# Kernel tuning notes

Measured on AMD Instinct MI355X. Metric: run time of the kernel, lower is better.

Reference implementation:

```python
import jax, jax.numpy as jnp
import numpy as np

D_PAIR = 128
D_BIAS = 128
N_HEAD = 4
D_HID = 32
B = 1
L = 384
EPS = 1e-5


def _layernorm(x, gamma, beta):
    m = jnp.mean(x, axis=-1, keepdims=True)
    v = jnp.var(x, axis=-1, keepdims=True)
    return (x - m) * jax.lax.rsqrt(v + EPS) * gamma + beta


def setup_inputs() -> dict:
    key = jax.random.key(0)
    ks = jax.random.split(key, 10)
    hd = N_HEAD * D_HID
    s = 0.02
    return {
        "pair": jax.random.normal(ks[0], (B, L, L, D_PAIR), jnp.float32),
        "bias": jax.random.normal(ks[1], (B, L, L, D_BIAS), jnp.float32),
        "gamma_p": jnp.ones((D_PAIR,), jnp.float32),
        "beta_p": jnp.zeros((D_PAIR,), jnp.float32),
        "gamma_b": jnp.ones((D_BIAS,), jnp.float32),
        "beta_b": jnp.zeros((D_BIAS,), jnp.float32),
        "Wq": jax.random.normal(ks[2], (D_PAIR, hd), jnp.float32) * s,
        "Wk": jax.random.normal(ks[3], (D_PAIR, hd), jnp.float32) * s,
        "Wv": jax.random.normal(ks[4], (D_PAIR, hd), jnp.float32) * s,
        "Wb": jax.random.normal(ks[5], (D_BIAS, N_HEAD), jnp.float32) * s,
        "Wg": jax.random.normal(ks[6], (D_PAIR, hd), jnp.float32) * s,
        "bg": jnp.ones((hd,), jnp.float32),
        "Wout": jax.random.normal(ks[7], (hd, D_PAIR), jnp.float32) * s,
        "bout": jnp.zeros((D_PAIR,), jnp.float32),
    }


def reference(pair, bias, gamma_p, beta_p, gamma_b, beta_b,
              Wq, Wk, Wv, Wb, Wg, bg, Wout, bout):
    h = Wb.shape[1]
    d = Wq.shape[1] // h
    Bn, Ln = pair.shape[:2]
    scaling = 1.0 / jnp.sqrt(jnp.asarray(d, pair.dtype))

    # is_row=True: attend along rows -> swap the two L axes
    pair_t = jnp.transpose(pair, (0, 2, 1, 3))
    bias_t = jnp.transpose(bias, (0, 2, 1, 3))

    pn = _layernorm(pair_t, gamma_p, beta_p)                     # [B,L,L,dp]
    q = (pn @ Wq).reshape(Bn, Ln, Ln, h, d) * scaling            # [B,n,i,h,d]
    k = (pn @ Wk).reshape(Bn, Ln, Ln, h, d) / Ln                 # [B,n,j,h,d]

    # mean-over-n biased axial attention logits: [B,i,j,h]
    attn = jnp.einsum('bnihk,bnjhk->bijh', q, k)
    attn = attn + _layernorm(bias_t, gamma_b, beta_b) @ Wb       # learned bias
    a = jax.nn.softmax(attn, axis=-2)                            # over j

    v = (pn @ Wv).reshape(Bn, Ln, Ln, h, d)                      # [B,n,j,h,d]
    o = jnp.einsum('bijh,bnjhd->bnihd', a, v).reshape(Bn, Ln, Ln, h * d)

    gate = jax.nn.sigmoid(pn @ Wg + bg)                          # [B,L,L,h*d]
    out = (gate * o) @ Wout + bout                               # [B,L,L,dp]

    return jnp.transpose(out, (0, 2, 1, 3))                      # undo is_row permute
```

## Files before the change

kernel.cpp:

```cpp
#include <hip/hip_runtime.h>

typedef unsigned short u16;
typedef unsigned int   u32;
typedef __attribute__((ext_vector_type(8))) short bf16x8;
typedef __attribute__((ext_vector_type(4))) float f32x4;

#define LL 384
#define DP 128
#define SZROW ((size_t)LL * LL)

#define SWZ(row, col) (((row) << 7) + (((((col) >> 3) ^ ((row) & 7)) << 3) | ((col) & 7)))

__device__ __forceinline__ u16 f2bf(float x) {
  u32 u = __builtin_bit_cast(u32, x);
  u = (u + 0x7FFFu + ((u >> 16) & 1u)) >> 16;
  return (u16)u;
}
__device__ __forceinline__ float bf2f(u16 h) {
  return __builtin_bit_cast(float, ((u32)h) << 16);
}
__device__ __forceinline__ uint2 pack4(float a, float b, float c, float d) {
  uint2 p;
  p.x = (u32)f2bf(a) | ((u32)f2bf(b) << 16);
  p.y = (u32)f2bf(c) | ((u32)f2bf(d) << 16);
  return p;
}

__global__ void k_prep(const float* __restrict__ Wq, const float* __restrict__ Wk,
                       const float* __restrict__ Wv, const float* __restrict__ Wg,
                       const float* __restrict__ Wout, u16* __restrict__ wbf) {
  int r = blockIdx.x, c = threadIdx.x, m = blockIdx.y;
  const float* W;
  float s = 1.0f;
  if (m == 0)      { W = Wq;  s = 0.17677669529663687f; }
  else if (m == 1) { W = Wk;  s = 1.0f / 384.0f; }
  else if (m == 2) { W = Wv; }
  else if (m == 3) { W = Wg; }
  else             { W = Wout; }
  wbf[m * DP * DP + r * DP + c] = f2bf(W[c * DP + r] * s);
}

template <int NS>
__device__ __forceinline__ void wave_gemm(const u16* __restrict__ W, const u16* pnl,
                                          int wave, int q, int r, f32x4 (&acc)[2][NS]) {
  const f32x4 FZ = {0.f, 0.f, 0.f, 0.f};
#pragma unroll
  for (int ms = 0; ms < 2; ++ms)
#pragma unroll
    for (int ns = 0; ns < NS; ++ns) acc[ms][ns] = FZ;
#pragma unroll
  for (int kc = 0; kc < 4; ++kc) {
    bf16x8 a0 = *(const bf16x8*)(W + (wave * 32 + r) * DP + kc * 32 + q * 8);
    bf16x8 a1 = *(const bf16x8*)(W + (wave * 32 + 16 + r) * DP + kc * 32 + q * 8);
#pragma unroll
    for (int ns = 0; ns < NS; ++ns) {
      bf16x8 b = *(const bf16x8*)(pnl + SWZ(ns * 16 + r, kc * 32 + q * 8));
      acc[0][ns] = __builtin_amdgcn_mfma_f32_16x16x32_bf16(a0, b, acc[0][ns], 0, 0, 0);
      acc[1][ns] = __builtin_amdgcn_mfma_f32_16x16x32_bf16(a1, b, acc[1][ns], 0, 0, 0);
    }
  }
}

__global__ __launch_bounds__(256) void k1_ln_proj(
    const float* __restrict__ pair, const float* __restrict__ gamma_p,
    const float* __restrict__ beta_p, const u16* __restrict__ wbf,
    const float* __restrict__ bg, u16* __restrict__ Qb, u16* __restrict__ Kb,
    u16* __restrict__ Vtb, u16* __restrict__ Gtb) {
  __shared__ u16 pn[64 * 128];
  __shared__ u16 T[128 * 72];
  const int ib = blockIdx.x, n = blockIdx.y;
  const int tid = threadIdx.x;
  const int lane = tid & 63, wave = tid >> 6;
  const int q = lane >> 4, r = lane & 15;
  const int l32 = lane & 31, half = lane >> 5;
  const int c0 = l32 * 4;
  const float4 gm = *(const float4*)(gamma_p + c0);
  const float4 bt = *(const float4*)(beta_p + c0);

#pragma unroll
  for (int it = 0; it < 8; ++it) {
    const int il = it * 8 + wave * 2 + half;
    const float* rowp = pair + ((size_t)(ib * 64 + il) * LL + n) * DP + c0;
    float4 x = *(const float4*)rowp;
    float s1 = x.x + x.y + x.z + x.w;
    float s2 = x.x * x.x + x.y * x.y + x.z * x.z + x.w * x.w;
#pragma unroll
    for (int m = 16; m >= 1; m >>= 1) { s1 += __shfl_xor(s1, m); s2 += __shfl_xor(s2, m); }
    float mean = s1 * (1.0f / 128.0f);
    float rs = rsqrtf(s2 * (1.0f / 128.0f) - mean * mean + 1e-5f);
    *(uint2*)(&pn[SWZ(il, c0)]) =
        pack4((x.x - mean) * rs * gm.x + bt.x, (x.y - mean) * rs * gm.y + bt.y,
              (x.z - mean) * rs * gm.z + bt.z, (x.w - mean) * rs * gm.w + bt.w);
  }
  __syncthreads();

  f32x4 acc[2][4];

  wave_gemm<4>(wbf, pn, wave, q, r, acc);
#pragma unroll
  for (int ms = 0; ms < 2; ++ms) {
    int ob = wave * 32 + ms * 16 + q * 4;
#pragma unroll
    for (int ns = 0; ns < 4; ++ns) {
      size_t base = ((size_t)n * LL + ib * 64 + ns * 16 + r) * DP + ob;
      *(uint2*)(Qb + base) = pack4(acc[ms][ns][0], acc[ms][ns][1], acc[ms][ns][2], acc[ms][ns][3]);
    }
  }
  wave_gemm<4>(wbf + DP * DP, pn, wave, q, r, acc);
#pragma unroll
  for (int ms = 0; ms < 2; ++ms) {
    int ob = wave * 32 + ms * 16 + q * 4;
#pragma unroll
    for (int ns = 0; ns < 4; ++ns) {
      size_t base = ((size_t)n * LL + ib * 64 + ns * 16 + r) * DP + ob;
      *(uint2*)(Kb + base) = pack4(acc[ms][ns][0], acc[ms][ns][1], acc[ms][ns][2], acc[ms][ns][3]);
    }
  }
  wave_gemm<4>(wbf + 2 * DP * DP, pn, wave, q, r, acc);
#pragma unroll
  for (int ms = 0; ms < 2; ++ms)
#pragma unroll
    for (int ns = 0; ns < 4; ++ns)
#pragma unroll
      for (int reg = 0; reg < 4; ++reg)
        T[(wave * 32 + ms * 16 + q * 4 + reg) * 72 + ns * 16 + r] = f2bf(acc[ms][ns][reg]);
  __syncthreads();
#pragma unroll
  for (int it = 0; it < 4; ++it) {
    int c = it * 32 + (tid >> 3);
    int il2 = (tid & 7) * 8;
    *(uint4*)(Vtb + ((size_t)n * DP + c) * LL + ib * 64 + il2) =
        *(const uint4*)(T + c * 72 + il2);
  }
  wave_gemm<4>(wbf + 3 * DP * DP, pn, wave, q, r, acc);
  __syncthreads();
#pragma unroll
  for (int ms = 0; ms < 2; ++ms) {
    f32x4 bgv = *(const f32x4*)(bg + wave * 32 + ms * 16 + q * 4);
#pragma unroll
    for (int ns = 0; ns < 4; ++ns)
#pragma unroll
      for (int reg = 0; reg < 4; ++reg) {
        float x = acc[ms][ns][reg] + bgv[reg];
        T[(wave * 32 + ms * 16 + q * 4 + reg) * 72 + ns * 16 + r] =
            f2bf(1.0f / (1.0f + __expf(-x)));
      }
  }
  __syncthreads();
#pragma unroll
  for (int it = 0; it < 4; ++it) {
    int c = it * 32 + (tid >> 3);
    int il2 = (tid & 7) * 8;
    *(uint4*)(Gtb + ((size_t)n * DP + c) * LL + ib * 64 + il2) =
        *(const uint4*)(T + c * 72 + il2);
  }
}

__global__ __launch_bounds__(256) void k2a_bias(
    const float* __restrict__ bias, const float* __restrict__ gamma_b,
    const float* __restrict__ beta_b, const float* __restrict__ Wb,
    float* __restrict__ part) {
  const int lane = threadIdx.x & 63, wave = threadIdx.x >> 6;
  const int l32 = lane & 31, half = lane >> 5;
  const int row = blockIdx.x * 8 + wave * 2 + half;
  const int i = row % LL, j = row / LL;
  const int c0 = l32 * 4;
  float4 x = *(const float4*)(bias + (size_t)row * DP + c0);
  float s1 = x.x + x.y + x.z + x.w;
  float s2 = x.x * x.x + x.y * x.y + x.z * x.z + x.w * x.w;
#pragma unroll
  for (int m = 16; m >= 1; m >>= 1) { s1 += __shfl_xor(s1, m); s2 += __shfl_xor(s2, m); }
  float mean = s1 * (1.0f / 128.0f);
  float rs = rsqrtf(s2 * (1.0f / 128.0f) - mean * mean + 1e-5f);
  const float4 gm = *(const float4*)(gamma_b + c0);
  const float4 bt = *(const float4*)(beta_b + c0);
  float y0 = (x.x - mean) * rs * gm.x + bt.x;
  float y1 = (x.y - mean) * rs * gm.y + bt.y;
  float y2 = (x.z - mean) * rs * gm.z + bt.z;
  float y3 = (x.w - mean) * rs * gm.w + bt.w;
  f32x4 w0 = *(const f32x4*)(Wb + (c0 + 0) * 4);
  f32x4 w1 = *(const f32x4*)(Wb + (c0 + 1) * 4);
  f32x4 w2 = *(const f32x4*)(Wb + (c0 + 2) * 4);
  f32x4 w3 = *(const f32x4*)(Wb + (c0 + 3) * 4);
  f32x4 pv = y0 * w0 + y1 * w1 + y2 * w2 + y3 * w3;
#pragma unroll
  for (int m = 16; m >= 1; m >>= 1) {
    pv[0] += __shfl_xor(pv[0], m); pv[1] += __shfl_xor(pv[1], m);
    pv[2] += __shfl_xor(pv[2], m); pv[3] += __shfl_xor(pv[3], m);
  }
  if (l32 == 0) {
    size_t o = (size_t)i * LL + j;
    part[(size_t)32 * SZROW + o] = pv[0];
    part[(size_t)33 * SZROW + o] = pv[1];
    part[(size_t)34 * SZROW + o] = pv[2];
    part[(size_t)35 * SZROW + o] = pv[3];
  }
}

__global__ __launch_bounds__(256) void k2b_qk(const u16* __restrict__ Qb,
                                              const u16* __restrict__ Kb,
                                              float* __restrict__ part) {
  const int it = blockIdx.y, jt = blockIdx.x >> 3, nc = blockIdx.x & 7;
  const int lane = threadIdx.x & 63, h = threadIdx.x >> 6;
  const int q = lane >> 4, r = lane & 15;
  const f32x4 FZ = {0.f, 0.f, 0.f, 0.f};
  f32x4 acc[3][3];
#pragma unroll
  for (int a = 0; a < 3; ++a)
#pragma unroll
    for (int b = 0; b < 3; ++b) acc[a][b] = FZ;
  const int coff = h * 32 + q * 8;
#pragma unroll 2
  for (int n = nc * 48; n < nc * 48 + 48; ++n) {
    const u16* Qp = Qb + ((size_t)n * LL + it * 48) * DP + coff;
    const u16* Kp = Kb + ((size_t)n * LL + jt * 48) * DP + coff;
    bf16x8 av[3], bv[3];
#pragma unroll
    for (int s = 0; s < 3; ++s) {
      av[s] = *(const bf16x8*)(Qp + (s * 16 + r) * DP);
      bv[s] = *(const bf16x8*)(Kp + (s * 16 + r) * DP);
    }
#pragma unroll
    for (int is = 0; is < 3; ++is)
#pragma unroll
      for (int js = 0; js < 3; ++js)
        acc[is][js] = __builtin_amdgcn_mfma_f32_16x16x32_bf16(av[is], bv[js], acc[is][js], 0, 0, 0);
  }
  float* dst = part + (size_t)(nc * 4 + h) * SZROW;
#pragma unroll
  for (int is = 0; is < 3; ++is)
#pragma unroll
    for (int js = 0; js < 3; ++js)
#pragma unroll
      for (int reg = 0; reg < 4; ++reg)
        dst[(size_t)(it * 48 + is * 16 + q * 4 + reg) * LL + jt * 48 + js * 16 + r] =
            acc[is][js][reg];
}

__global__ __launch_bounds__(384) void k3_softmax(const float* __restrict__ part,
                                                  u16* __restrict__ abf) {
  const int i = blockIdx.x, h = blockIdx.y, j = threadIdx.x;
  __shared__ float red[6];
  float l = 0.f;
#pragma unroll
  for (int c = 0; c < 9; ++c) l += part[(size_t)(c * 4 + h) * SZROW + (size_t)i * LL + j];
  float m = l;
#pragma unroll
  for (int s = 32; s >= 1; s >>= 1) m = fmaxf(m, __shfl_xor(m, s));
  const int wv = threadIdx.x >> 6;
  if ((threadIdx.x & 63) == 0) red[wv] = m;
  __syncthreads();
  m = fmaxf(fmaxf(fmaxf(red[0], red[1]), fmaxf(red[2], red[3])), fmaxf(red[4], red[5]));
  float e = __expf(l - m);
  float s = e;
#pragma unroll
  for (int t = 32; t >= 1; t >>= 1) s += __shfl_xor(s, t);
  __syncthreads();
  if ((threadIdx.x & 63) == 0) red[wv] = s;
  __syncthreads();
  s = red[0] + red[1] + red[2] + red[3] + red[4] + red[5];
  abf[((size_t)h * LL + i) * LL + j] = f2bf(e / s);
}

__global__ __launch_bounds__(256) void k4_out(
    const u16* __restrict__ abf, const u16* __restrict__ Vtb,
    const u16* __restrict__ Gtb, const u16* __restrict__ Wot,
    const float* __restrict__ bout, float* __restrict__ out) {
  __shared__ u16 go[64 * 128];
  const int n = blockIdx.x, ib = blockIdx.y;
  const int lane = threadIdx.x & 63, wave = threadIdx.x >> 6;
  const int h = wave;
  const int q = lane >> 4, r = lane & 15;

  uint2 gp[4][2];
#pragma unroll
  for (int is = 0; is < 4; ++is)
#pragma unroll
    for (int ds = 0; ds < 2; ++ds) {
      int c = h * 32 + ds * 16 + r;
      gp[is][ds] =
          *(const uint2*)(Gtb + ((size_t)n * DP + c) * LL + ib * 64 + is * 16 + q * 4);
    }

  const f32x4 FZ = {0.f, 0.f, 0.f, 0.f};
  f32x4 acc[4][2];
#pragma unroll
  for (int is = 0; is < 4; ++is) { acc[is][0] = FZ; acc[is][1] = FZ; }

  const u16* Vbase = Vtb + ((size_t)n * DP + h * 32) * LL;
  const u16* Abase = abf + ((size_t)h * LL + ib * 64) * LL;
#pragma unroll
  for (int halfk = 0; halfk < 2; ++halfk) {
    bf16x8 vb[6][2];
#pragma unroll
    for (int k2 = 0; k2 < 6; ++k2) {
      const u16* Vp = Vbase + (halfk * 6 + k2) * 32 + q * 8;
      vb[k2][0] = *(const bf16x8*)(Vp + (size_t)r * LL);
      vb[k2][1] = *(const bf16x8*)(Vp + (size_t)(16 + r) * LL);
    }
#pragma unroll
    for (int k2 = 0; k2 < 6; ++k2) {
      const int kc = halfk * 6 + k2;
#pragma unroll
      for (int is = 0; is < 4; ++is) {
        bf16x8 a = *(const bf16x8*)(Abase + (size_t)(is * 16 + r) * LL + kc * 32 + q * 8);
        acc[is][0] = __builtin_amdgcn_mfma_f32_16x16x32_bf16(a, vb[k2][0], acc[is][0], 0, 0, 0);
        acc[is][1] = __builtin_amdgcn_mfma_f32_16x16x32_bf16(a, vb[k2][1], acc[is][1], 0, 0, 0);
      }
    }
  }
#pragma unroll
  for (int is = 0; is < 4; ++is)
#pragma unroll
    for (int ds = 0; ds < 2; ++ds) {
      int c = h * 32 + ds * 16 + r;
      float g0 = bf2f((u16)(gp[is][ds].x & 0xffff)), g1 = bf2f((u16)(gp[is][ds].x >> 16));
      float g2 = bf2f((u16)(gp[is][ds].y & 0xffff)), g3 = bf2f((u16)(gp[is][ds].y >> 16));
      int il = is * 16 + q * 4;
      go[SWZ(il + 0, c)] = f2bf(g0 * acc[is][ds][0]);
      go[SWZ(il + 1, c)] = f2bf(g1 * acc[is][ds][1]);
      go[SWZ(il + 2, c)] = f2bf(g2 * acc[is][ds][2]);
      go[SWZ(il + 3, c)] = f2bf(g3 * acc[is][ds][3]);
    }
  __syncthreads();

  f32x4 acc2[2][4];
  wave_gemm<4>(Wot, go, wave, q, r, acc2);
#pragma unroll
  for (int ms = 0; ms < 2; ++ms) {
    int co = wave * 32 + ms * 16 + q * 4;
    f32x4 bo = *(const f32x4*)(bout + co);
#pragma unroll
    for (int ns = 0; ns < 4; ++ns) {
      f32x4 v = acc2[ms][ns] + bo;
      *(f32x4*)(out + ((size_t)(ib * 64 + ns * 16 + r) * LL + n) * DP + co) = v;
    }
  }
}

extern "C" void kernel_launch(void* const* d_in, const int* in_sizes, int n_in,
                              void* d_out, int out_size, void* d_ws, size_t ws_size,
                              hipStream_t stream) {
  const float* pair    = (const float*)d_in[0];
  const float* bias    = (const float*)d_in[1];
  const float* gamma_p = (const float*)d_in[2];
  const float* beta_p  = (const float*)d_in[3];
  const float* gamma_b = (const float*)d_in[4];
  const float* beta_b  = (const float*)d_in[5];
  const float* Wq      = (const float*)d_in[6];
  const float* Wk      = (const float*)d_in[7];
  const float* Wv      = (const float*)d_in[8];
  const float* Wb      = (const float*)d_in[9];
  const float* Wg      = (const float*)d_in[10];
  const float* bg      = (const float*)d_in[11];
  const float* Wout    = (const float*)d_in[12];
  const float* bout    = (const float*)d_in[13];

  u16* Qb = (u16*)d_out;
  u16* Kb = Qb + (size_t)LL * LL * DP;

  char* ws = (char*)d_ws;
  const size_t BF_PLANE = (size_t)LL * LL * DP * 2;
  u16*   Vtb  = (u16*)ws;
  u16*   Gtb  = (u16*)(ws + BF_PLANE);
  float* part = (float*)(ws + 2 * BF_PLANE);
  u16*   abf  = (u16*)(ws + 2 * BF_PLANE + 36 * SZROW * 4);
  u16*   wbf  = (u16*)(ws + 2 * BF_PLANE + 36 * SZROW * 4 + 4 * SZROW * 2);
  float* out  = (float*)d_out;

  k_prep<<<dim3(128, 5), 128, 0, stream>>>(Wq, Wk, Wv, Wg, Wout, wbf);
  k1_ln_proj<<<dim3(6, 384), 256, 0, stream>>>(pair, gamma_p, beta_p, wbf, bg, Qb, Kb, Vtb, Gtb);
  k2a_bias<<<dim3(18432), 256, 0, stream>>>(bias, gamma_b, beta_b, Wb, part);
  k2b_qk<<<dim3(64, 8), 256, 0, stream>>>(Qb, Kb, part);
  k3_softmax<<<dim3(384, 4), 384, 0, stream>>>(part, abf);
  k4_out<<<dim3(384, 6), 256, 0, stream>>>(abf, Vtb, Gtb, wbf + 4 * DP * DP, bout, out);
}
```

Measured before the change: 470.0 us.

## Repack Q/K/V/attention into per-head k-chunk tiles and stage output through LDS

Q and K are now stored head-major as [n][h][L][32], so each MFMA fragment load in the QK kernel reads contiguous 64-byte rows instead of striding by 128 channels. V and the softmax probabilities are written in 32-wide k-chunk tiles, which makes the A/V loads in the output kernel contiguous, and the A fragments are double-buffered across k chunks. The output tile is staged through shared memory so each row is written to global memory as full coalesced 512-byte lines instead of scattered 16-byte pieces. The cost is an extra shared-memory pass and barrier in the output kernel, plus more registers for the prefetch buffers.

```diff
diff --git a/kernel.cpp b/kernel.cpp
--- a/kernel.cpp
+++ b/kernel.cpp
@@ -25,6 +25,7 @@
   p.y = (u32)f2bf(c) | ((u32)f2bf(d) << 16);
   return p;
 }
+
 
 __global__ void k_prep(const float* __restrict__ Wq, const float* __restrict__ Wk,
                        const float* __restrict__ Wv, const float* __restrict__ Wg,
@@ -65,7 +66,7 @@
     const float* __restrict__ pair, const float* __restrict__ gamma_p,
     const float* __restrict__ beta_p, const u16* __restrict__ wbf,
     const float* __restrict__ bg, u16* __restrict__ Qb, u16* __restrict__ Kb,
-    u16* __restrict__ Vtb, u16* __restrict__ Gtb) {
+    u16* __restrict__ Vp, u16* __restrict__ Gtb) {
   __shared__ u16 pn[64 * 128];
   __shared__ u16 T[128 * 72];
   const int ib = blockIdx.x, n = blockIdx.y;
@@ -99,20 +100,18 @@
   wave_gemm<4>(wbf, pn, wave, q, r, acc);
 #pragma unroll
   for (int ms = 0; ms < 2; ++ms) {
-    int ob = wave * 32 + ms * 16 + q * 4;
 #pragma unroll
     for (int ns = 0; ns < 4; ++ns) {
-      size_t base = ((size_t)n * LL + ib * 64 + ns * 16 + r) * DP + ob;
+      size_t base = (((size_t)n * 4 + wave) * LL + ib * 64 + ns * 16 + r) * 32 + ms * 16 + q * 4;
       *(uint2*)(Qb + base) = pack4(acc[ms][ns][0], acc[ms][ns][1], acc[ms][ns][2], acc[ms][ns][3]);
     }
   }
   wave_gemm<4>(wbf + DP * DP, pn, wave, q, r, acc);
 #pragma unroll
   for (int ms = 0; ms < 2; ++ms) {
-    int ob = wave * 32 + ms * 16 + q * 4;
 #pragma unroll
     for (int ns = 0; ns < 4; ++ns) {
-      size_t base = ((size_t)n * LL + ib * 64 + ns * 16 + r) * DP + ob;
+      size_t base = (((size_t)n * 4 + wave) * LL + ib * 64 + ns * 16 + r) * 32 + ms * 16 + q * 4;
       *(uint2*)(Kb + base) = pack4(acc[ms][ns][0], acc[ms][ns][1], acc[ms][ns][2], acc[ms][ns][3]);
     }
   }
@@ -126,11 +125,14 @@
         T[(wave * 32 + ms * 16 + q * 4 + reg) * 72 + ns * 16 + r] = f2bf(acc[ms][ns][reg]);
   __syncthreads();
 #pragma unroll
-  for (int it = 0; it < 4; ++it) {
-    int c = it * 32 + (tid >> 3);
-    int il2 = (tid & 7) * 8;
-    *(uint4*)(Vtb + ((size_t)n * DP + c) * LL + ib * 64 + il2) =
-        *(const uint4*)(T + c * 72 + il2);
+  for (int kk = 0; kk < 2; ++kk) {
+    u16* dst = Vp + ((size_t)n * 12 + ib * 2 + kk) * (128 * 32);
+#pragma unroll
+    for (int e = 0; e < 2; ++e) {
+      int m = e * 256 + tid;
+      int c = m >> 2, io = (m & 3) * 8;
+      *(uint4*)(dst + c * 32 + io) = *(const uint4*)(T + c * 72 + kk * 32 + io);
+    }
   }
   wave_gemm<4>(wbf + 3 * DP * DP, pn, wave, q, r, acc);
   __syncthreads();
@@ -209,16 +211,15 @@
   for (int a = 0; a < 3; ++a)
 #pragma unroll
     for (int b = 0; b < 3; ++b) acc[a][b] = FZ;
-  const int coff = h * 32 + q * 8;
 #pragma unroll 2
   for (int n = nc * 48; n < nc * 48 + 48; ++n) {
-    const u16* Qp = Qb + ((size_t)n * LL + it * 48) * DP + coff;
-    const u16* Kp = Kb + ((size_t)n * LL + jt * 48) * DP + coff;
+    const u16* Qp = Qb + (((size_t)n * 4 + h) * LL + it * 48 + r) * 32 + q * 8;
+    const u16* Kp = Kb + (((size_t)n * 4 + h) * LL + jt * 48 + r) * 32 + q * 8;
     bf16x8 av[3], bv[3];
 #pragma unroll
     for (int s = 0; s < 3; ++s) {
-      av[s] = *(const bf16x8*)(Qp + (s * 16 + r) * DP);
-      bv[s] = *(const bf16x8*)(Kp + (s * 16 + r) * DP);
+      av[s] = *(const bf16x8*)(Qp + s * 16 * 32);
+      bv[s] = *(const bf16x8*)(Kp + s * 16 * 32);
     }
 #pragma unroll
     for (int is = 0; is < 3; ++is)
@@ -238,7 +239,7 @@
 }
 
 __global__ __launch_bounds__(384) void k3_softmax(const float* __restrict__ part,
-                                                  u16* __restrict__ abf) {
+                                                  u16* __restrict__ ap) {
   const int i = blockIdx.x, h = blockIdx.y, j = threadIdx.x;
   __shared__ float red[6];
   float l = 0.f;
@@ -259,16 +260,19 @@
   if ((threadIdx.x & 63) == 0) red[wv] = s;
   __syncthreads();
   s = red[0] + red[1] + red[2] + red[3] + red[4] + red[5];
-  abf[((size_t)h * LL + i) * LL + j] = f2bf(e / s);
+  ap[(((size_t)h * 12 + (j >> 5)) * LL + i) * 32 + (j & 31)] = f2bf(e / s);
 }
 
 __global__ __launch_bounds__(256) void k4_out(
-    const u16* __restrict__ abf, const u16* __restrict__ Vtb,
+    const u16* __restrict__ ap, const u16* __restrict__ Vp,
     const u16* __restrict__ Gtb, const u16* __restrict__ Wot,
     const float* __restrict__ bout, float* __restrict__ out) {
-  __shared__ u16 go[64 * 128];
+  __shared__ __align__(16) char smem[64 * 132 * 4];
+  u16*   go = (u16*)smem;
+  float* O  = (float*)smem;
   const int n = blockIdx.x, ib = blockIdx.y;
-  const int lane = threadIdx.x & 63, wave = threadIdx.x >> 6;
+  const int tid = threadIdx.x;
+  const int lane = tid & 63, wave = tid >> 6;
   const int h = wave;
   const int q = lane >> 4, r = lane & 15;
 
@@ -287,25 +291,35 @@
 #pragma unroll
   for (int is = 0; is < 4; ++is) { acc[is][0] = FZ; acc[is][1] = FZ; }
 
-  const u16* Vbase = Vtb + ((size_t)n * DP + h * 32) * LL;
-  const u16* Abase = abf + ((size_t)h * LL + ib * 64) * LL;
+  const u16* Vbase = Vp + (size_t)n * 12 * (128 * 32) + (h * 32 + r) * 32 + q * 8;
+  const u16* Abase = ap + ((size_t)h * 12 * LL + ib * 64 + r) * 32 + q * 8;
+
+  bf16x8 av[2][4];
+#pragma unroll
+  for (int is = 0; is < 4; ++is) av[0][is] = *(const bf16x8*)(Abase + (size_t)is * 16 * 32);
+
 #pragma unroll
   for (int halfk = 0; halfk < 2; ++halfk) {
     bf16x8 vb[6][2];
 #pragma unroll
     for (int k2 = 0; k2 < 6; ++k2) {
-      const u16* Vp = Vbase + (halfk * 6 + k2) * 32 + q * 8;
-      vb[k2][0] = *(const bf16x8*)(Vp + (size_t)r * LL);
-      vb[k2][1] = *(const bf16x8*)(Vp + (size_t)(16 + r) * LL);
+      const u16* Vkc = Vbase + (size_t)(halfk * 6 + k2) * (128 * 32);
+      vb[k2][0] = *(const bf16x8*)(Vkc);
+      vb[k2][1] = *(const bf16x8*)(Vkc + 16 * 32);
     }
 #pragma unroll
     for (int k2 = 0; k2 < 6; ++k2) {
       const int kc = halfk * 6 + k2;
+      const int cur = kc & 1, nxt = cur ^ 1;
+      if (kc < 11) {
+        const u16* An = Abase + (size_t)(kc + 1) * LL * 32;
+#pragma unroll
+        for (int is = 0; is < 4; ++is) av[nxt][is] = *(const bf16x8*)(An + (size_t)is * 16 * 32);
+      }
 #pragma unroll
       for (int is = 0; is < 4; ++is) {
-        bf16x8 a = *(const bf16x8*)(Abase + (size_t)(is * 16 + r) * LL + kc * 32 + q * 8);
-        acc[is][0] = __builtin_amdgcn_mfma_f32_16x16x32_bf16(a, vb[k2][0], acc[is][0], 0, 0, 0);
-        acc[is][1] = __builtin_amdgcn_mfma_f32_16x16x32_bf16(a, vb[k2][1], acc[is][1], 0, 0, 0);
+        acc[is][0] = __builtin_amdgcn_mfma_f32_16x16x32_bf16(av[cur][is], vb[k2][0], acc[is][0], 0, 0, 0);
+        acc[is][1] = __builtin_amdgcn_mfma_f32_16x16x32_bf16(av[cur][is], vb[k2][1], acc[is][1], 0, 0, 0);
       }
     }
   }
@@ -326,15 +340,23 @@
 
   f32x4 acc2[2][4];
   wave_gemm<4>(Wot, go, wave, q, r, acc2);
+  __syncthreads();
+
 #pragma unroll
   for (int ms = 0; ms < 2; ++ms) {
     int co = wave * 32 + ms * 16 + q * 4;
     f32x4 bo = *(const f32x4*)(bout + co);
 #pragma unroll
-    for (int ns = 0; ns < 4; ++ns) {
-      f32x4 v = acc2[ms][ns] + bo;
-      *(f32x4*)(out + ((size_t)(ib * 64 + ns * 16 + r) * LL + n) * DP + co) = v;
-    }
+    for (int ns = 0; ns < 4; ++ns)
+      *(f32x4*)(O + (ns * 16 + r) * 132 + co) = acc2[ms][ns] + bo;
+  }
+  __syncthreads();
+#pragma unroll
+  for (int e = 0; e < 8; ++e) {
+    int m = e * 256 + tid;
+    int il = m >> 5, cw = (m & 31) * 4;
+    *(f32x4*)(out + ((size_t)(ib * 64 + il) * LL + n) * DP + cw) =
+        *(const f32x4*)(O + il * 132 + cw);
   }
 }
 
@@ -361,17 +383,17 @@
 
   char* ws = (char*)d_ws;
   const size_t BF_PLANE = (size_t)LL * LL * DP * 2;
-  u16*   Vtb  = (u16*)ws;
+  u16*   Vp   = (u16*)ws;
   u16*   Gtb  = (u16*)(ws + BF_PLANE);
   float* part = (float*)(ws + 2 * BF_PLANE);
-  u16*   abf  = (u16*)(ws + 2 * BF_PLANE + 36 * SZROW * 4);
+  u16*   ap   = (u16*)(ws + 2 * BF_PLANE + 36 * SZROW * 4);
   u16*   wbf  = (u16*)(ws + 2 * BF_PLANE + 36 * SZROW * 4 + 4 * SZROW * 2);
   float* out  = (float*)d_out;
 
   k_prep<<<dim3(128, 5), 128, 0, stream>>>(Wq, Wk, Wv, Wg, Wout, wbf);
-  k1_ln_proj<<<dim3(6, 384), 256, 0, stream>>>(pair, gamma_p, beta_p, wbf, bg, Qb, Kb, Vtb, Gtb);
+  k1_ln_proj<<<dim3(6, 384), 256, 0, stream>>>(pair, gamma_p, beta_p, wbf, bg, Qb, Kb, Vp, Gtb);
   k2a_bias<<<dim3(18432), 256, 0, stream>>>(bias, gamma_b, beta_b, Wb, part);
   k2b_qk<<<dim3(64, 8), 256, 0, stream>>>(Qb, Kb, part);
-  k3_softmax<<<dim3(384, 4), 384, 0, stream>>>(part, abf);
-  k4_out<<<dim3(384, 6), 256, 0, stream>>>(abf, Vtb, Gtb, wbf + 4 * DP * DP, bout, out);
-}
+  k3_softmax<<<dim3(384, 4), 384, 0, stream>>>(part, ap);
+  k4_out<<<dim3(384, 6), 256, 0, stream>>>(ap, Vp, Gtb, wbf + 4 * DP * DP, bout, out);
+}
```

After: 395.9 us. 1.19x faster.
